# Performance work log

Measured on AMD Instinct MI355X. Metric: run time of the kernel, lower is better.

## Reference

```python
import jax, jax.numpy as jnp
from jax import lax
import numpy as np

TAO = 12   # lag stride
M = 7      # number of lags (m)


def setup_inputs() -> dict:
    key = jax.random.key(0)
    k1, k2, k3, k4, k5 = jax.random.split(key, 5)
    B, L, C, D = 32, 4096, 21, 512
    K = D // C            # kernels per channel = 24
    LO = D - C * K        # leftout channels = 8
    return {
        "x": jax.random.normal(k1, (B, L, C), jnp.float32),
        "conv_w": jax.random.normal(k2, (K, M + 1, 3), jnp.float32) * 0.2,
        "conv_b": jax.random.normal(k3, (K,), jnp.float32) * 0.02,
        "leftout_w": jax.random.normal(k4, (LO, M + 1, 3), jnp.float32) * 0.2,
        "leftout_b": jax.random.normal(k5, (LO,), jnp.float32) * 0.02,
    }


def _circ_conv(x_ncl, w_oik, b_o):
    # circular padding=1, kernel_size=3, stride 1 -> same length
    xp = jnp.pad(x_ncl, ((0, 0), (0, 0), (1, 1)), mode="wrap")
    y = lax.conv_general_dilated(xp, w_oik, (1,), "VALID",
                                 dimension_numbers=("NCW", "OIW", "NCW"))
    return y + b_o[None, :, None]


def reference(x, conv_w, conv_b, leftout_w, leftout_b):
    B, L, C = x.shape
    K = conv_w.shape[0]
    nv = L - M * TAO
    # lagged gather: ext[b, t, c, j] = x[b, m*tao + t - j*tao, c]
    t_idx = jnp.arange(M * TAO, L)                      # [nv]
    offs = jnp.arange(M + 1) * TAO                      # [m+1]
    idx = t_idx[:, None] - offs[None, :]                # [nv, m+1]
    ext = x[:, idx, :]                                  # [B, nv, m+1, C]
    ext = jnp.transpose(ext, (0, 1, 3, 2))              # [B, nv, C, m+1] (channel-major)
    # pad=True: zero-pad the first m*tao timesteps
    ext = jnp.pad(ext, ((0, 0), (M * TAO, 0), (0, 0), (0, 0)))  # [B, L, C, m+1]
    # per-channel chunks as a single batched conv: [B*C, m+1, L]
    xc = jnp.transpose(ext, (0, 2, 3, 1)).reshape(B * C, M + 1, L)
    y = _circ_conv(xc, conv_w, conv_b).reshape(B, C * K, L)      # [B, C*K, L]
    # leftout conv applied to the last channel's chunk only
    last = jnp.transpose(ext[:, :, C - 1, :], (0, 2, 1))         # [B, m+1, L]
    yl = _circ_conv(last, leftout_w, leftout_b)                  # [B, LO, L]
    out = jnp.concatenate([y, yl], axis=1)                       # [B, d_model, L]
    return jnp.transpose(out, (0, 2, 1))                         # [B, L, d_model]
```

## Files before the change

kernel.cpp:

```cpp
#include <hip/hip_runtime.h>

#define LL 4096
#define CC 21
#define TT 64
#define NTB 2
#define XSTR 151
#define STG_N (150 * CC)
#define NSTG 13

typedef float v2f __attribute__((ext_vector_type(2)));
typedef float v4f __attribute__((ext_vector_type(4)));

__device__ __forceinline__ v2f fma2(v2f a, v2f b, v2f c) {
    return __builtin_elementwise_fma(a, b, c);
}

__device__ __forceinline__ void prefetch_tile(const float* __restrict__ xb,
                                              int baset, int tid, float* pf) {
    const int lo21 = (0 - baset) * CC;
    const int hi21 = (LL - baset) * CC;
    #pragma unroll
    for (int i = 0; i < NSTG; ++i) {
        int e = tid + 256 * i;
        if (e < STG_N) {
            int ofs = baset * CC + e;
            if (e < lo21)  ofs += LL * CC;
            if (e >= hi21) ofs -= LL * CC;
            pf[i] = xb[ofs];
        }
    }
}

__device__ __forceinline__ void write_tile(float* __restrict__ xsb, int tid,
                                           const int* ldsoff, const float* pf) {
    #pragma unroll
    for (int i = 0; i < NSTG; ++i) {
        int e = tid + 256 * i;
        if (e < STG_N) xsb[ldsoff[i]] = pf[i];
    }
}

template<bool EDGE>
__device__ __forceinline__ void compute_item(
    const float* __restrict__ xrow, const float* __restrict__ wtc,
    const float* __restrict__ biasc, float* __restrict__ outp,
    int vo0, int d0, int tg, int t0)
{
    v2f acc[16][2];
    {
        v2f b0 = { biasc[vo0],     biasc[vo0 + 1] };
        v2f b1 = { biasc[vo0 + 2], biasc[vo0 + 3] };
        #pragma unroll
        for (int ti = 0; ti < 16; ++ti) { acc[ti][0] = b0; acc[ti][1] = b1; }
    }

    bool msk[18];
    if (EDGE) {
        #pragma unroll
        for (int s = 0; s < 18; ++s)
            msk[s] = (((t0 + tg * 16 + s - 1) & (LL - 1)) < 84);
    }

    const int base = tg * 16 + 84;

    #pragma unroll 1
    for (int j = 0; j < 8; ++j) {
        const float* wp = &wtc[(3 * j) * 32 + vo0];
        float4 w0 = *reinterpret_cast<const float4*>(wp);
        float4 w1 = *reinterpret_cast<const float4*>(wp + 32);
        float4 w2 = *reinterpret_cast<const float4*>(wp + 64);

        const float* vp = xrow + base - 12 * j;
        float v[18];
        #pragma unroll
        for (int s = 0; s < 18; ++s) {
            float t = vp[s];
            if (EDGE && msk[s]) t = 0.0f;
            v[s] = t;
        }

        #pragma unroll
        for (int ti = 0; ti < 16; ++ti) {
            v2f vv, w;
            vv.x = vv.y = v[ti];
            w.x = w0.x; w.y = w0.y; acc[ti][0] = fma2(vv, w, acc[ti][0]);
            w.x = w0.z; w.y = w0.w; acc[ti][1] = fma2(vv, w, acc[ti][1]);
            vv.x = vv.y = v[ti + 1];
            w.x = w1.x; w.y = w1.y; acc[ti][0] = fma2(vv, w, acc[ti][0]);
            w.x = w1.z; w.y = w1.w; acc[ti][1] = fma2(vv, w, acc[ti][1]);
            vv.x = vv.y = v[ti + 2];
            w.x = w2.x; w.y = w2.y; acc[ti][0] = fma2(vv, w, acc[ti][0]);
            w.x = w2.z; w.y = w2.w; acc[ti][1] = fma2(vv, w, acc[ti][1]);
        }
    }

    #pragma unroll
    for (int ti = 0; ti < 16; ++ti) {
        v4f r = { acc[ti][0].x, acc[ti][0].y, acc[ti][1].x, acc[ti][1].y };
        float* p = outp + (size_t)(tg * 16 + ti) * 512 + d0;
        *reinterpret_cast<v4f*>(p) = r;
    }
}

__global__ __launch_bounds__(256) void delay_fir_kernel(
    const float* __restrict__ x,
    const float* __restrict__ conv_w,
    const float* __restrict__ conv_b,
    const float* __restrict__ lw,
    const float* __restrict__ lb,
    float* __restrict__ out)
{
    __shared__ float xs[2][CC * XSTR];
    __shared__ __align__(16) float wtc[24 * 32];
    __shared__ float biasc[32];

    const int tid   = threadIdx.x;
    const int b     = blockIdx.y;
    const int tbase = blockIdx.x * (TT * NTB);

    for (int e = tid; e < 24 * 32; e += 256) {
        int jk = e >> 5, vo = e & 31;
        wtc[e] = (vo < 24) ? conv_w[vo * 24 + jk] : lw[(vo - 24) * 24 + jk];
    }
    if (tid < 32) biasc[tid] = (tid < 24) ? conv_b[tid] : lb[tid - 24];

    const float* xb = x + (size_t)b * (LL * CC);

    int ldsoff[NSTG];
    #pragma unroll
    for (int i = 0; i < NSTG; ++i) {
        int e = tid + 256 * i;
        int s = e / CC, c2 = e - s * CC;
        ldsoff[i] = c2 * XSTR + s;
    }

    const int l  = tid & 63;
    const int w  = tid >> 6;
    const int d0 = 256 * (w & 1) + 4 * l;
    int c, vo0;
    if (d0 >= 504) { c = 20; vo0 = 24 + (d0 - 504); }
    else           { c = d0 / 24; vo0 = d0 - c * 24; }

    float pf[NSTG];
    prefetch_tile(xb, tbase - 85, tid, pf);
    write_tile(xs[0], tid, ldsoff, pf);
    __syncthreads();

    #pragma unroll 1
    for (int tix = 0; tix < NTB; ++tix) {
        const int t0 = tbase + tix * TT;
        const float* xrow = &xs[tix & 1][c * XSTR];

        if (tix + 1 < NTB) prefetch_tile(xb, t0 + TT - 85, tid, pf);

        float* outp = out + ((size_t)b * LL + t0) * 512;
        const bool edge = (t0 == 0) | (t0 == TT) | (t0 == LL - TT);
        #pragma unroll 1
        for (int it = 0; it < 2; ++it) {
            int tg = it * 2 + (w >> 1);
            if (edge) compute_item<true >(xrow, wtc, biasc, outp, vo0, d0, tg, t0);
            else      compute_item<false>(xrow, wtc, biasc, outp, vo0, d0, tg, t0);
        }

        if (tix + 1 < NTB) {
            write_tile(xs[(tix + 1) & 1], tid, ldsoff, pf);
            __syncthreads();
        }
    }
}

extern "C" void kernel_launch(void* const* d_in, const int* in_sizes, int n_in,
                              void* d_out, int out_size, void* d_ws, size_t ws_size,
                              hipStream_t stream) {
    const float* x      = (const float*)d_in[0];
    const float* conv_w = (const float*)d_in[1];
    const float* conv_b = (const float*)d_in[2];
    const float* lw     = (const float*)d_in[3];
    const float* lb     = (const float*)d_in[4];
    float* out = (float*)d_out;

    dim3 grid(LL / (TT * NTB), 32);
    delay_fir_kernel<<<grid, 256, 0, stream>>>(x, conv_w, conv_b, lw, lb, out);
}
```

Baseline: 62.28 us.

## Vectorize LDS row reads with padded stride and lighter barriers

Pads the LDS row stride to a multiple of four and aligns the shared tile so each thread can read its 18 input samples with four 128-bit and one 64-bit LDS loads instead of 18 scalar loads. The 13 precomputed LDS store offsets are dropped and recomputed inline, which frees registers at the cost of extra integer work. __syncthreads is replaced by a raw lgkmcnt wait plus s_barrier, skipping the vmcnt wait. Edge masking is applied after the vector load.

New measurement: 62.24 us. Within noise of the previous version (-0.1%).

```diff
diff --git a/kernel.cpp b/kernel.cpp
--- a/kernel.cpp
+++ b/kernel.cpp
@@ -4,7 +4,7 @@
 #define CC 21
 #define TT 64
 #define NTB 2
-#define XSTR 151
+#define XSTR 156
 #define STG_N (150 * CC)
 #define NSTG 13
 
@@ -14,6 +14,11 @@
 __device__ __forceinline__ v2f fma2(v2f a, v2f b, v2f c) {
     return __builtin_elementwise_fma(a, b, c);
 }
+
+#define RAW_BARRIER() do {                                  \
+    asm volatile("s_waitcnt lgkmcnt(0)" ::: "memory");      \
+    __builtin_amdgcn_s_barrier();                           \
+} while (0)
 
 __device__ __forceinline__ void prefetch_tile(const float* __restrict__ xb,
                                               int baset, int tid, float* pf) {
@@ -32,11 +37,14 @@
 }
 
 __device__ __forceinline__ void write_tile(float* __restrict__ xsb, int tid,
-                                           const int* ldsoff, const float* pf) {
+                                           const float* pf) {
     #pragma unroll
     for (int i = 0; i < NSTG; ++i) {
         int e = tid + 256 * i;
-        if (e < STG_N) xsb[ldsoff[i]] = pf[i];
+        if (e < STG_N) {
+            int s = e / CC, c2 = e - s * CC;
+            xsb[c2 * XSTR + s] = pf[i];
+        }
     }
 }
 
@@ -65,18 +73,23 @@
 
     #pragma unroll 1
     for (int j = 0; j < 8; ++j) {
-        const float* wp = &wtc[(3 * j) * 32 + vo0];
-        float4 w0 = *reinterpret_cast<const float4*>(wp);
-        float4 w1 = *reinterpret_cast<const float4*>(wp + 32);
-        float4 w2 = *reinterpret_cast<const float4*>(wp + 64);
+        const float* wp = &wtc[96 * j + vo0];
+        v4f w0 = *reinterpret_cast<const v4f*>(wp);
+        v4f w1 = *reinterpret_cast<const v4f*>(wp + 32);
+        v4f w2 = *reinterpret_cast<const v4f*>(wp + 64);
 
-        const float* vp = xrow + base - 12 * j;
-        float v[18];
-        #pragma unroll
-        for (int s = 0; s < 18; ++s) {
-            float t = vp[s];
-            if (EDGE && msk[s]) t = 0.0f;
-            v[s] = t;
+        const float* vp = xrow + (base - 12 * j);
+        v4f va = *reinterpret_cast<const v4f*>(vp);
+        v4f vb = *reinterpret_cast<const v4f*>(vp + 4);
+        v4f vc = *reinterpret_cast<const v4f*>(vp + 8);
+        v4f vd = *reinterpret_cast<const v4f*>(vp + 12);
+        v2f ve = *reinterpret_cast<const v2f*>(vp + 16);
+        float v[18] = { va.x, va.y, va.z, va.w, vb.x, vb.y, vb.z, vb.w,
+                        vc.x, vc.y, vc.z, vc.w, vd.x, vd.y, vd.z, vd.w,
+                        ve.x, ve.y };
+        if (EDGE) {
+            #pragma unroll
+            for (int s = 0; s < 18; ++s) if (msk[s]) v[s] = 0.0f;
         }
 
         #pragma unroll
@@ -110,7 +123,7 @@
     const float* __restrict__ lb,
     float* __restrict__ out)
 {
-    __shared__ float xs[2][CC * XSTR];
+    __shared__ __align__(16) float xs[2][CC * XSTR];
     __shared__ __align__(16) float wtc[24 * 32];
     __shared__ float biasc[32];
 
@@ -126,14 +139,6 @@
 
     const float* xb = x + (size_t)b * (LL * CC);
 
-    int ldsoff[NSTG];
-    #pragma unroll
-    for (int i = 0; i < NSTG; ++i) {
-        int e = tid + 256 * i;
-        int s = e / CC, c2 = e - s * CC;
-        ldsoff[i] = c2 * XSTR + s;
-    }
-
     const int l  = tid & 63;
     const int w  = tid >> 6;
     const int d0 = 256 * (w & 1) + 4 * l;
@@ -143,8 +148,8 @@
 
     float pf[NSTG];
     prefetch_tile(xb, tbase - 85, tid, pf);
-    write_tile(xs[0], tid, ldsoff, pf);
-    __syncthreads();
+    write_tile(xs[0], tid, pf);
+    RAW_BARRIER();
 
     #pragma unroll 1
     for (int tix = 0; tix < NTB; ++tix) {
@@ -163,8 +168,8 @@
         }
 
         if (tix + 1 < NTB) {
-            write_tile(xs[(tix + 1) & 1], tid, ldsoff, pf);
-            __syncthreads();
+            write_tile(xs[(tix + 1) & 1], tid, pf);
+            RAW_BARRIER();
         }
     }
 }
```
